# Optimization experiments

Measured on AMD Instinct MI355X. Metric: run time of the kernel, lower is better.

The kernel has to match this reference:

```python
import jax, jax.numpy as jnp
import numpy as np

VOCAB = 100000
EMB = 256
HID = 512
HH = HID // 2  # per-direction hidden
NTAGS = 12
START = 10
STOP = 11
SEQ = 2048
NEG = -10000.0


def setup_inputs() -> dict:
    key = jax.random.key(0)
    ks = jax.random.split(key, 18)
    s = 0.05
    inp = {
        "sentence": jax.random.randint(ks[0], (SEQ,), 0, VOCAB, dtype=jnp.int64 if jax.config.jax_enable_x64 else jnp.int32),
        "tags": jax.random.randint(ks[1], (SEQ,), 0, 10, dtype=jnp.int64 if jax.config.jax_enable_x64 else jnp.int32),
        "embed": jax.random.normal(ks[2], (VOCAB, EMB), jnp.float32) * s,
        "Wih_f": jax.random.normal(ks[3], (4 * HH, EMB), jnp.float32) * s,
        "Whh_f": jax.random.normal(ks[4], (4 * HH, HH), jnp.float32) * s,
        "bih_f": jax.random.normal(ks[5], (4 * HH,), jnp.float32) * s,
        "bhh_f": jax.random.normal(ks[6], (4 * HH,), jnp.float32) * s,
        "Wih_b": jax.random.normal(ks[7], (4 * HH, EMB), jnp.float32) * s,
        "Whh_b": jax.random.normal(ks[8], (4 * HH, HH), jnp.float32) * s,
        "bih_b": jax.random.normal(ks[9], (4 * HH,), jnp.float32) * s,
        "bhh_b": jax.random.normal(ks[10], (4 * HH,), jnp.float32) * s,
        "W_out": jax.random.normal(ks[11], (NTAGS, HID), jnp.float32) * s,
        "b_out": jax.random.normal(ks[12], (NTAGS,), jnp.float32) * s,
        "h0": jax.random.normal(ks[14], (2, HH), jnp.float32),
        "c0": jax.random.normal(ks[15], (2, HH), jnp.float32),
    }
    trans = jax.random.normal(ks[13], (NTAGS, NTAGS), jnp.float32)
    trans = trans.at[START, :].set(NEG)  # never transition INTO start
    trans = trans.at[:, STOP].set(NEG)   # never transition FROM stop
    inp["transitions"] = trans
    return inp


def _lstm_dir(x, h0, c0, Wih, Whh, bih, bhh):
    # x: [T, E]; PyTorch gate order i, f, g, o
    pre = x @ Wih.T + bih + bhh  # [T, 4*HH] precomputed input projection
    def step(carry, p):
        h, c = carry
        g = p + Whh @ h
        i, f, gg, o = jnp.split(g, 4)
        i = jax.nn.sigmoid(i)
        f = jax.nn.sigmoid(f)
        gg = jnp.tanh(gg)
        o = jax.nn.sigmoid(o)
        c = f * c + i * gg
        h = o * jnp.tanh(c)
        return (h, c), h
    _, hs = jax.lax.scan(step, (h0, c0), pre)
    return hs  # [T, HH]


def _forward_impl(sentence, tags, embed, Wih_f, Whh_f, bih_f, bhh_f,
                  Wih_b, Whh_b, bih_b, bhh_b, W_out, b_out, transitions, h0, c0):
    x = embed[sentence]  # [T, E]
    hf = _lstm_dir(x, h0[0], c0[0], Wih_f, Whh_f, bih_f, bhh_f)
    hb = jnp.flip(_lstm_dir(jnp.flip(x, 0), h0[1], c0[1], Wih_b, Whh_b, bih_b, bhh_b), 0)
    feats = jnp.concatenate([hf, hb], axis=-1) @ W_out.T + b_out  # [T, NTAGS]

    # CRF forward algorithm: log-semiring scan over time
    fv0 = jnp.full((NTAGS,), NEG, feats.dtype).at[START].set(0.0)
    def crf_step(fv, emit):
        # transitions[next, prev]; logsumexp over prev
        fv = jax.nn.logsumexp(fv[None, :] + transitions + emit[:, None], axis=1)
        return fv, None
    fv, _ = jax.lax.scan(crf_step, fv0, feats)
    forward_score = jax.nn.logsumexp(fv + transitions[STOP])

    # gold path score
    prev = jnp.concatenate([jnp.array([START], dtype=tags.dtype), tags[:-1]])
    emit_gold = jnp.take_along_axis(feats, tags[:, None], axis=1)[:, 0]
    gold_score = jnp.sum(transitions[tags, prev]) + jnp.sum(emit_gold) + transitions[STOP, tags[-1]]

    return forward_score - gold_score


def reference(sentence, tags, embed, Wih_f, Whh_f, bih_f, bhh_f,
              Wih_b, Whh_b, bih_b, bhh_b, W_out, b_out, transitions, h0, c0):
    return _forward_impl(sentence, tags, embed, Wih_f, Whh_f, bih_f, bhh_f,
                         Wih_b, Whh_b, bih_b, bhh_b, W_out, b_out, transitions, h0, c0)
```

## Files before the change

### kernel.cpp

```cpp
#include <hip/hip_runtime.h>
#include <hip/hip_bf16.h>
#include <stdint.h>

#define SEQ   2048
#define EMB   256
#define HHD   256
#define GATES 1024
#define NTAGS 12
#define START 10
#define STOP  11
#define CCH   16
#define CLEN  128

__device__ __forceinline__ int sdot4(uint32_t a, uint32_t b, int c) {
#if __has_builtin(__builtin_amdgcn_sdot4)
  return __builtin_amdgcn_sdot4((int)a, (int)b, c, false);
#else
  int r = c;
#pragma unroll
  for (int i = 0; i < 4; i++) {
    int av = (int)(signed char)((a >> (8 * i)) & 255);
    int bv = (int)(signed char)((b >> (8 * i)) & 255);
    r += av * bv;
  }
  return r;
#endif
}

__device__ __forceinline__ float fsig(float x) {
  float e = __expf(-x);
  return __builtin_amdgcn_rcpf(1.0f + e);
}

__device__ __forceinline__ int dpp_xor1(int x) {
  return __builtin_amdgcn_update_dpp(0, x, 0xB1, 0xF, 0xF, true);
}
__device__ __forceinline__ int dpp_xor2(int x) {
  return __builtin_amdgcn_update_dpp(0, x, 0x4E, 0xF, 0xF, true);
}
__device__ __forceinline__ float dpp_xor2_f(float x) {
  int r = __builtin_amdgcn_update_dpp(0, __float_as_int(x), 0x4E, 0xF, 0xF, true);
  return __int_as_float(r);
}

__global__ __launch_bounds__(256) void k_front(const float* __restrict__ whh_f,
                                               const float* __restrict__ whh_b,
                                               uint32_t* __restrict__ q4,
                                               float* __restrict__ scales,
                                               const int* __restrict__ sentence,
                                               const float* __restrict__ embed,
                                               const float* __restrict__ Wih_f,
                                               const float* __restrict__ bih_f,
                                               const float* __restrict__ bhh_f,
                                               const float* __restrict__ Wih_b,
                                               const float* __restrict__ bih_b,
                                               const float* __restrict__ bhh_b,
                                               float* __restrict__ pre) {
  if (blockIdx.x < 512) {
    const int row  = (blockIdx.x * 256 + threadIdx.x) >> 6;
    const int lane = threadIdx.x & 63;
    const int d = row >> 10, r = row & 1023;
    const float4 w = *(const float4*)((d ? whh_b : whh_f) + (long)r * HHD + lane * 4);
    float m = fmaxf(fmaxf(fabsf(w.x), fabsf(w.y)), fmaxf(fabsf(w.z), fabsf(w.w)));
#pragma unroll
    for (int off = 32; off; off >>= 1) m = fmaxf(m, __shfl_xor(m, off, 64));
    m = fmaxf(m, 1e-20f);
    const float inv = 127.f / m;
    int a = (int)rintf(w.x * inv), b = (int)rintf(w.y * inv);
    int c = (int)rintf(w.z * inv), e = (int)rintf(w.w * inv);
    q4[row * 64 + lane] = (uint32_t)(a & 255) | ((uint32_t)(b & 255) << 8) |
                          ((uint32_t)(c & 255) << 16) | ((uint32_t)(e & 255) << 24);
    if (lane == 0) scales[row] = m / 127.f;
    return;
  }
  const int bid2 = blockIdx.x - 512;
  const int dir  = bid2 >> 8;
  const int t0   = (bid2 & 255) * 8;
  const float* Wih = dir ? Wih_b : Wih_f;
  const float* bih = dir ? bih_b : bih_f;
  const float* bhh = dir ? bhh_b : bhh_f;

  __shared__ float xs[8][256];
  const int uu = threadIdx.x;
#pragma unroll
  for (int i = 0; i < 8; i++) {
    int s = sentence[t0 + i];
    xs[i][uu] = embed[(long)s * EMB + uu];
  }
  __syncthreads();

  float acc[4][8];
#pragma unroll
  for (int j = 0; j < 4; j++)
#pragma unroll
    for (int t = 0; t < 8; t++) acc[j][t] = 0.f;

  const float4* W4 = (const float4*)Wih;
#pragma unroll
  for (int j = 0; j < 4; j++) {
    const float4* Wrow = W4 + (long)(j * 256 + uu) * 64;
    for (int kq = 0; kq < 64; kq++) {
      const float4 w = Wrow[kq];
#pragma unroll
      for (int t = 0; t < 8; t++) {
        const float4 xv = ((const float4*)xs[t])[kq];
        acc[j][t] += w.x * xv.x + w.y * xv.y + w.z * xv.z + w.w * xv.w;
      }
    }
  }
  float bs[4];
#pragma unroll
  for (int j = 0; j < 4; j++) bs[j] = bih[j * 256 + uu] + bhh[j * 256 + uu];
#pragma unroll
  for (int t = 0; t < 8; t++) {
    float4 o = {acc[0][t] + bs[0], acc[1][t] + bs[1],
                acc[2][t] + bs[2], acc[3][t] + bs[3]};
    *(float4*)&pre[(((long)(dir * SEQ + t0 + t)) * HHD + uu) * 4] = o;
  }
}

__global__ __launch_bounds__(512, 2) void k_lstm(const uint32_t* __restrict__ q4,
                                                 const float* __restrict__ scales,
                                                 const float* __restrict__ pre,
                                                 const float* __restrict__ h0,
                                                 const float* __restrict__ c0,
                                                 float* __restrict__ hs) {
  const int dir  = blockIdx.x;
  const int L    = threadIdx.x;
  const int q    = L & 3;
  const int g    = L >> 2;
  const int p    = q & 1;
  const int half = q >> 1;
  const int u    = 2 * g + p;

  __shared__ __align__(16) uint8_t hbuf[2][256];

  const long base = (long)dir * GATES;

  uint4 wa[4][4], wb[4][4];
  const uint4* qq = (const uint4*)q4;
#pragma unroll
  for (int j = 0; j < 4; j++) {
    const int qj = q ^ j;
    const int rA = (2 * (qj >> 1)) * 256 + 2 * g + (qj & 1);
    const int rB = rA + 256;
#pragma unroll
    for (int k = 0; k < 4; k++) {
      wa[j][k] = qq[(base + rA) * 16 + 4 * q + k];
      wb[j][k] = qq[(base + rB) * 16 + 4 * q + k];
    }
  }
  const int rown = (2 * half) * 256 + u;
  const float sA = scales[base + rown];
  const float sB = scales[base + rown + 256];

  if (L < 256) {
    float v = h0[dir * HHD + L] * (127.f / 4.f);
    v = fminf(fmaxf(v, -127.f), 127.f);
    hbuf[0][L] = (uint8_t)(int)rintf(v);
  }
  float c_st = c0[dir * HHD + u];
  __syncthreads();

  const int t0 = dir ? (SEQ - 1) : 0;
  const long pstep = dir ? -(long)(HHD * 4) : (long)(HHD * 4);
  const long hstep = dir ? -(long)HHD : (long)HHD;
  const float* pp = pre + (long)dir * SEQ * (HHD * 4) + ((long)t0 * HHD + u) * 4 + 2 * half;
  float* hp       = hs  + (long)dir * SEQ * HHD + (long)t0 * HHD + u;
  const float gmul = half ? 2.f : 1.f;
  const int write_h = ((L & 2) == 0);

  for (int s = 0; s < SEQ; s++) {
    const float2 pr = *(const float2*)pp;

    const uint4* hq4 = (const uint4*)(hbuf[s & 1] + (q << 6));
    const uint4 h0v = hq4[0], h1v = hq4[1], h2v = hq4[2], h3v = hq4[3];

    int pa0 = 0, pa1 = 0, pa2 = 0, pa3 = 0;
    int pb0 = 0, pb1 = 0, pb2 = 0, pb3 = 0;
#pragma unroll
    for (int k = 0; k < 4; k++) {
      const uint4 hk = (k == 0) ? h0v : (k == 1) ? h1v : (k == 2) ? h2v : h3v;
      pa0 = sdot4(wa[0][k].x, hk.x, pa0); pa0 = sdot4(wa[0][k].y, hk.y, pa0);
      pa0 = sdot4(wa[0][k].z, hk.z, pa0); pa0 = sdot4(wa[0][k].w, hk.w, pa0);
      pa1 = sdot4(wa[1][k].x, hk.x, pa1); pa1 = sdot4(wa[1][k].y, hk.y, pa1);
      pa1 = sdot4(wa[1][k].z, hk.z, pa1); pa1 = sdot4(wa[1][k].w, hk.w, pa1);
      pa2 = sdot4(wa[2][k].x, hk.x, pa2); pa2 = sdot4(wa[2][k].y, hk.y, pa2);
      pa2 = sdot4(wa[2][k].z, hk.z, pa2); pa2 = sdot4(wa[2][k].w, hk.w, pa2);
      pa3 = sdot4(wa[3][k].x, hk.x, pa3); pa3 = sdot4(wa[3][k].y, hk.y, pa3);
      pa3 = sdot4(wa[3][k].z, hk.z, pa3); pa3 = sdot4(wa[3][k].w, hk.w, pa3);
      pb0 = sdot4(wb[0][k].x, hk.x, pb0); pb0 = sdot4(wb[0][k].y, hk.y, pb0);
      pb0 = sdot4(wb[0][k].z, hk.z, pb0); pb0 = sdot4(wb[0][k].w, hk.w, pb0);
      pb1 = sdot4(wb[1][k].x, hk.x, pb1); pb1 = sdot4(wb[1][k].y, hk.y, pb1);
      pb1 = sdot4(wb[1][k].z, hk.z, pb1); pb1 = sdot4(wb[1][k].w, hk.w, pb1);
      pb2 = sdot4(wb[2][k].x, hk.x, pb2); pb2 = sdot4(wb[2][k].y, hk.y, pb2);
      pb2 = sdot4(wb[2][k].z, hk.z, pb2); pb2 = sdot4(wb[2][k].w, hk.w, pb2);
      pb3 = sdot4(wb[3][k].x, hk.x, pb3); pb3 = sdot4(wb[3][k].y, hk.y, pb3);
      pb3 = sdot4(wb[3][k].z, hk.z, pb3); pb3 = sdot4(wb[3][k].w, hk.w, pb3);
    }
    const int tA = pa0 + dpp_xor1(pa1);
    const int tA2 = pa2 + dpp_xor1(pa3);
    const int sumA = tA + dpp_xor2(tA2);
    const int tB = pb0 + dpp_xor1(pb1);
    const int tB2 = pb2 + dpp_xor1(pb3);
    const int sumB = tB + dpp_xor2(tB2);

    const float hsc = (s == 0) ? (4.f / 127.f) : (1.f / 127.f);
    const float gA = pr.x + sA * hsc * (float)sumA;
    const float gB = pr.y + sB * hsc * (float)sumB;

    const float v0 = fsig(gA * gmul) * gmul - (gmul - 1.f);
    const float v1 = fsig(gB);
    const float p0 = dpp_xor2_f(v0);
    const float p1 = dpp_xor2_f(v1);
    const float iv = half ? p0 : v0;
    const float fv = half ? p1 : v1;
    const float gv = half ? v0 : p0;
    const float ov = half ? v1 : p1;

    c_st = fv * c_st + iv * gv;
    const float hv = ov * (2.f * fsig(2.f * c_st) - 1.f);

    if (write_h) {
      *hp = hv;
      hbuf[(s + 1) & 1][u] = (uint8_t)(int)rintf(hv * 127.f);
    }
    pp += pstep;
    hp += hstep;
    __syncthreads();
  }
}

__global__ __launch_bounds__(1024) void k_tail(const float* __restrict__ hs,
                                               const float* __restrict__ W_out,
                                               const float* __restrict__ b_out,
                                               const float* __restrict__ trans,
                                               float* __restrict__ feats,
                                               float* __restrict__ Pc) {
  const int ch  = blockIdx.x;
  const int tid = threadIdx.x;

  __shared__ float Wl[12 * 520];
  __shared__ float fe[CLEN * NTAGS];
  for (int i = tid; i < 12 * 512; i += 1024) Wl[(i / 512) * 520 + (i % 512)] = W_out[i];
  __syncthreads();

  for (int idx = tid; idx < CLEN * NTAGS; idx += 1024) {
    const int tl = idx / 12, n = idx % 12;
    const int t  = ch * CLEN + tl;
    const float4* hf4 = (const float4*)(hs + (long)t * HHD);
    const float4* hb4 = (const float4*)(hs + (long)SEQ * HHD + (long)t * HHD);
    const float4* Wa  = (const float4*)&Wl[n * 520];
    const float4* Wb  = (const float4*)&Wl[n * 520 + 256];
    float acc = b_out[n];
#pragma unroll 8
    for (int j = 0; j < 64; j++) {
      float4 w = Wa[j], h = hf4[j];
      acc += w.x * h.x + w.y * h.y + w.z * h.z + w.w * h.w;
    }
#pragma unroll 8
    for (int j = 0; j < 64; j++) {
      float4 w = Wb[j], h = hb4[j];
      acc += w.x * h.x + w.y * h.y + w.z * h.z + w.w * h.w;
    }
    fe[tl * NTAGS + n] = acc;
    feats[t * NTAGS + n] = acc;
  }
  __syncthreads();

  if (tid < 192) {
    const int n   = tid & 15;
    const int p   = tid >> 4;
    const int nn  = (n < 12) ? n : 11;

    float trn[12];
#pragma unroll
    for (int j = 0; j < 12; j++) trn[j] = trans[nn * 12 + j];

    float Mv = trn[p] + fe[nn];
    for (int t = 1; t < CLEN; t++) {
      float x[12], m = -1e30f;
#pragma unroll
      for (int j = 0; j < 12; j++) {
        x[j] = trn[j] + __shfl(Mv, (tid & 48) | j, 64);
        m = fmaxf(m, x[j]);
      }
      float ss = 0.f;
#pragma unroll
      for (int j = 0; j < 12; j++) ss += __expf(x[j] - m);
      Mv = fe[t * NTAGS + nn] + m + __logf(ss);
    }
    if (n < 12) Pc[ch * 144 + n * 12 + p] = Mv;
  }
}

__global__ __launch_bounds__(128) void k_crf_final(const float* __restrict__ Pc,
                                                   const float* __restrict__ feats,
                                                   const int* __restrict__ tags,
                                                   const float* __restrict__ trans,
                                                   float* __restrict__ out) {
  __shared__ float Pl[CCH * 144];
  __shared__ float res[2];
  const int tid = threadIdx.x;
  for (int i = tid; i < CCH * 144; i += 128) Pl[i] = Pc[i];
  __syncthreads();

  if (tid < 64) {
    const int n  = tid;
    const int nn = (n < 12) ? n : 11;
    float fv = (n == START) ? 0.f : -10000.f;
    for (int c = 0; c < CCH; c++) {
      float x[12], m = -1e30f;
#pragma unroll
      for (int j = 0; j < 12; j++) {
        x[j] = Pl[c * 144 + nn * 12 + j] + __shfl(fv, j, 64);
        m = fmaxf(m, x[j]);
      }
      float ss = 0.f;
#pragma unroll
      for (int j = 0; j < 12; j++) ss += __expf(x[j] - m);
      fv = m + __logf(ss);
    }
    const float v = fv + trans[STOP * 12 + nn];
    float xs[12], m = -1e30f;
#pragma unroll
    for (int j = 0; j < 12; j++) {
      xs[j] = __shfl(v, j, 64);
      m = fmaxf(m, xs[j]);
    }
    float ss = 0.f;
#pragma unroll
    for (int j = 0; j < 12; j++) ss += __expf(xs[j] - m);
    if (tid == 0) res[0] = m + __logf(ss);
  } else {
    const int i = tid - 64;
    float gp = 0.f;
    for (int b = 0; b < 32; b++) {
      int t  = b * 64 + i;
      int tg = tags[t];
      int pv = (t == 0) ? START : tags[t - 1];
      gp += trans[tg * 12 + pv] + feats[t * NTAGS + tg];
    }
#pragma unroll
    for (int off = 32; off; off >>= 1) gp += __shfl_xor(gp, off, 64);
    if (i == 0) res[1] = gp + trans[STOP * 12 + tags[SEQ - 1]];
  }
  __syncthreads();
  if (tid == 0) out[0] = res[0] - res[1];
}

extern "C" void kernel_launch(void* const* d_in, const int* in_sizes, int n_in,
                              void* d_out, int out_size, void* d_ws, size_t ws_size,
                              hipStream_t stream) {
  const int*   sentence = (const int*)  d_in[0];
  const int*   tags     = (const int*)  d_in[1];
  const float* embed    = (const float*)d_in[2];
  const float* Wih_f    = (const float*)d_in[3];
  const float* Whh_f    = (const float*)d_in[4];
  const float* bih_f    = (const float*)d_in[5];
  const float* bhh_f    = (const float*)d_in[6];
  const float* Wih_b    = (const float*)d_in[7];
  const float* Whh_b    = (const float*)d_in[8];
  const float* bih_b    = (const float*)d_in[9];
  const float* bhh_b    = (const float*)d_in[10];
  const float* W_out    = (const float*)d_in[11];
  const float* b_out    = (const float*)d_in[12];
  const float* h0       = (const float*)d_in[13];
  const float* c0       = (const float*)d_in[14];
  const float* trans    = (const float*)d_in[15];
  float* out = (float*)d_out;

  char* ws = (char*)d_ws;
  uint32_t* q4    = (uint32_t*)ws;
  float*    scales= (float*)(ws + (512l << 10));
  float*    pre   = (float*)(ws + (1l  << 20));
  float*    hs    = (float*)(ws + (17l << 20));
  float*    feats = (float*)(ws + (21l << 20));
  float*    Pc    = (float*)(ws + (21l << 20) + (128l<<10));

  k_front<<<1024, 256, 0, stream>>>(Whh_f, Whh_b, q4, scales,
                                    sentence, embed, Wih_f, bih_f, bhh_f,
                                    Wih_b, bih_b, bhh_b, pre);
  k_lstm<<<2, 512, 0, stream>>>(q4, scales, pre, h0, c0, hs);
  k_tail<<<CCH, 1024, 0, stream>>>(hs, W_out, b_out, trans, feats, Pc);
  k_crf_final<<<1, 128, 0, stream>>>(Pc, feats, tags, trans, out);
}
```

Baseline: 1.798 ms.

## Fuse CRF final reduction into tail kernel via last-block atomic counter

Removes the separate single-block CRF final kernel. Each tail block now computes its chunk's gold-path partial score from the shared-memory emissions, and the last block to finish, detected with an atomic counter reset in the front kernel, combines the chunk matrices and gold partials. This saves one kernel launch and the global write and read of the feats array. In exchange it adds a threadfence and atomic handshake, and the final reduction runs serially after the slowest block.

```diff
diff --git a/kernel.cpp b/kernel.cpp
--- a/kernel.cpp
+++ b/kernel.cpp
@@ -55,7 +55,9 @@
                                                const float* __restrict__ Wih_b,
                                                const float* __restrict__ bih_b,
                                                const float* __restrict__ bhh_b,
-                                               float* __restrict__ pre) {
+                                               float* __restrict__ pre,
+                                               unsigned int* __restrict__ cnt) {
+  if (blockIdx.x == 0 && threadIdx.x == 0) *cnt = 0;
   if (blockIdx.x < 512) {
     const int row  = (blockIdx.x * 256 + threadIdx.x) >> 6;
     const int lane = threadIdx.x & 63;
@@ -235,13 +237,18 @@
                                                const float* __restrict__ W_out,
                                                const float* __restrict__ b_out,
                                                const float* __restrict__ trans,
-                                               float* __restrict__ feats,
-                                               float* __restrict__ Pc) {
+                                               const int* __restrict__ tags,
+                                               float* __restrict__ Pc,
+                                               float* __restrict__ Gc,
+                                               unsigned int* __restrict__ cnt,
+                                               float* __restrict__ out) {
   const int ch  = blockIdx.x;
   const int tid = threadIdx.x;
 
   __shared__ float Wl[12 * 520];
   __shared__ float fe[CLEN * NTAGS];
+  __shared__ float gpart[2];
+  __shared__ int   sh_last;
   for (int i = tid; i < 12 * 512; i += 1024) Wl[(i / 512) * 520 + (i % 512)] = W_out[i];
   __syncthreads();
 
@@ -264,7 +271,6 @@
       acc += w.x * h.x + w.y * h.y + w.z * h.z + w.w * h.w;
     }
     fe[tl * NTAGS + n] = acc;
-    feats[t * NTAGS + n] = acc;
   }
   __syncthreads();
 
@@ -292,61 +298,69 @@
     }
     if (n < 12) Pc[ch * 144 + n * 12 + p] = Mv;
   }
-}
-
-__global__ __launch_bounds__(128) void k_crf_final(const float* __restrict__ Pc,
-                                                   const float* __restrict__ feats,
-                                                   const int* __restrict__ tags,
-                                                   const float* __restrict__ trans,
-                                                   float* __restrict__ out) {
-  __shared__ float Pl[CCH * 144];
-  __shared__ float res[2];
-  const int tid = threadIdx.x;
-  for (int i = tid; i < CCH * 144; i += 128) Pl[i] = Pc[i];
-  __syncthreads();
-
-  if (tid < 64) {
-    const int n  = tid;
-    const int nn = (n < 12) ? n : 11;
-    float fv = (n == START) ? 0.f : -10000.f;
-    for (int c = 0; c < CCH; c++) {
-      float x[12], m = -1e30f;
+  else if (tid >= 256 && tid < 384) {
+    const int tl = tid - 256;
+    const int t  = ch * CLEN + tl;
+    const int tg = tags[t];
+    const int pv = (t == 0) ? START : tags[t - 1];
+    float gv = trans[tg * 12 + pv] + fe[tl * NTAGS + tg];
+#pragma unroll
+    for (int off = 32; off; off >>= 1) gv += __shfl_xor(gv, off, 64);
+    if ((tid & 63) == 0) gpart[(tid >> 6) - 4] = gv;
+  }
+  __syncthreads();
+
+  if (tid == 0) {
+    float gc = gpart[0] + gpart[1];
+    if (ch == CCH - 1) gc += trans[STOP * 12 + tags[SEQ - 1]];
+    Gc[ch] = gc;
+    __threadfence();
+    unsigned int old = __hip_atomic_fetch_add(cnt, 1u, __ATOMIC_ACQ_REL,
+                                              __HIP_MEMORY_SCOPE_AGENT);
+    sh_last = (old == CCH - 1);
+  }
+  __syncthreads();
+
+  if (sh_last) {
+    __shared__ float Pl[CCH * 144];
+    __shared__ float res[2];
+    for (int i = tid; i < CCH * 144; i += 1024) Pl[i] = Pc[i];
+    if (tid == 64) {
+      float gs = 0.f;
+#pragma unroll
+      for (int c = 0; c < CCH; c++) gs += Gc[c];
+      res[1] = gs;
+    }
+    __syncthreads();
+    if (tid < 64) {
+      const int n  = tid;
+      const int nn = (n < 12) ? n : 11;
+      float fv = (n == START) ? 0.f : -10000.f;
+      for (int c = 0; c < CCH; c++) {
+        float x[12], m = -1e30f;
+#pragma unroll
+        for (int j = 0; j < 12; j++) {
+          x[j] = Pl[c * 144 + nn * 12 + j] + __shfl(fv, j, 64);
+          m = fmaxf(m, x[j]);
+        }
+        float ss = 0.f;
+#pragma unroll
+        for (int j = 0; j < 12; j++) ss += __expf(x[j] - m);
+        fv = m + __logf(ss);
+      }
+      const float v = fv + trans[STOP * 12 + nn];
+      float xs[12], m = -1e30f;
 #pragma unroll
       for (int j = 0; j < 12; j++) {
-        x[j] = Pl[c * 144 + nn * 12 + j] + __shfl(fv, j, 64);
-        m = fmaxf(m, x[j]);
+        xs[j] = __shfl(v, j, 64);
+        m = fmaxf(m, xs[j]);
       }
       float ss = 0.f;
 #pragma unroll
-      for (int j = 0; j < 12; j++) ss += __expf(x[j] - m);
-      fv = m + __logf(ss);
-    }
-    const float v = fv + trans[STOP * 12 + nn];
-    float xs[12], m = -1e30f;
-#pragma unroll
-    for (int j = 0; j < 12; j++) {
-      xs[j] = __shfl(v, j, 64);
-      m = fmaxf(m, xs[j]);
-    }
-    float ss = 0.f;
-#pragma unroll
-    for (int j = 0; j < 12; j++) ss += __expf(xs[j] - m);
-    if (tid == 0) res[0] = m + __logf(ss);
-  } else {
-    const int i = tid - 64;
-    float gp = 0.f;
-    for (int b = 0; b < 32; b++) {
-      int t  = b * 64 + i;
-      int tg = tags[t];
-      int pv = (t == 0) ? START : tags[t - 1];
-      gp += trans[tg * 12 + pv] + feats[t * NTAGS + tg];
-    }
-#pragma unroll
-    for (int off = 32; off; off >>= 1) gp += __shfl_xor(gp, off, 64);
-    if (i == 0) res[1] = gp + trans[STOP * 12 + tags[SEQ - 1]];
-  }
-  __syncthreads();
-  if (tid == 0) out[0] = res[0] - res[1];
+      for (int j = 0; j < 12; j++) ss += __expf(xs[j] - m);
+      if (tid == 0) out[0] = (m + __logf(ss)) - res[1];
+    }
+  }
 }
 
 extern "C" void kernel_launch(void* const* d_in, const int* in_sizes, int n_in,
@@ -375,13 +389,13 @@
   float*    scales= (float*)(ws + (512l << 10));
   float*    pre   = (float*)(ws + (1l  << 20));
   float*    hs    = (float*)(ws + (17l << 20));
-  float*    feats = (float*)(ws + (21l << 20));
-  float*    Pc    = (float*)(ws + (21l << 20) + (128l<<10));
+  float*    Pc    = (float*)(ws + (21l << 20));
+  float*    Gc    = (float*)(ws + (21l << 20) + (16l<<10));
+  unsigned* cnt   = (unsigned*)(ws + (21l << 20) + (32l<<10));
 
   k_front<<<1024, 256, 0, stream>>>(Whh_f, Whh_b, q4, scales,
                                     sentence, embed, Wih_f, bih_f, bhh_f,
-                                    Wih_b, bih_b, bhh_b, pre);
+                                    Wih_b, bih_b, bhh_b, pre, cnt);
   k_lstm<<<2, 512, 0, stream>>>(q4, scales, pre, h0, c0, hs);
-  k_tail<<<CCH, 1024, 0, stream>>>(hs, W_out, b_out, trans, feats, Pc);
-  k_crf_final<<<1, 128, 0, stream>>>(Pc, feats, tags, trans, out);
-}
+  k_tail<<<CCH, 1024, 0, stream>>>(hs, W_out, b_out, trans, tags, Pc, Gc, cnt, out);
+}
```

Measured after the change: 1.796 ms. No clear change (-0.1%).
